# Performance work log

Hardware: AMD Instinct MI355X
Metric: run time of the kernel (lower is better)

## Reference

```python
import jax, jax.numpy as jnp
import numpy as np

NUM_HEADS = 8
EPS = 1e-12  # matches torch F.normalize default eps


def setup_inputs() -> dict:
    key = jax.random.key(0)
    k1, k2 = jax.random.split(key)
    x = jax.random.normal(k1, (8, 384, 128, 128), dtype=jnp.float32)
    # 1x1 conv weight [out=3*dim, in=dim]
    w_qkv = jax.random.normal(k2, (1152, 384), dtype=jnp.float32) * (1.0 / np.sqrt(384))
    return {"x": x, "w_qkv": w_qkv}


def _l2norm(t):
    # torch F.normalize(dim=-1): x / max(||x||2, eps)
    n = jnp.sqrt(jnp.sum(t * t, axis=-1, keepdims=True))
    return t / jnp.maximum(n, EPS)


def reference(x, w_qkv):
    B, C, H, W = x.shape
    hw = H * W
    head_c = C // NUM_HEADS
    # 1x1 conv == channel matmul
    qkv = jnp.einsum('bchw,oc->bohw', x, w_qkv)  # [B, 3C, H, W]
    q, k, v = jnp.split(qkv, 3, axis=1)
    def rs(t):
        return t.reshape(B, NUM_HEADS, head_c, hw)
    q, k, v = rs(q), rs(k), rs(v)
    q = _l2norm(q)
    k = _l2norm(k)
    scale = jnp.sqrt(jnp.float32(hw))
    attn = jnp.einsum('bhcn,bhdn->bhcd', q, k) / scale  # small CxC per head
    attn = jax.nn.softmax(attn, axis=-1)
    out = jnp.einsum('bhcd,bhdn->bhcn', attn, v)
    return out.reshape(B, C, H, W)
```

## Files before the change

### kernel.cpp

```cpp
#include <hip/hip_runtime.h>

typedef short short8 __attribute__((ext_vector_type(8)));
typedef __bf16 bf16x8 __attribute__((ext_vector_type(8)));
typedef float f32x4 __attribute__((ext_vector_type(4)));
typedef int i32x4 __attribute__((ext_vector_type(4)));

typedef const __attribute__((address_space(1))) void* gas_p;
typedef __attribute__((address_space(3))) void* las_p;

static __device__ __forceinline__ unsigned short f2bf(float f) {
  unsigned u = __builtin_bit_cast(unsigned, f);
  u += 0x7fffu + ((u >> 16) & 1u);
  return (unsigned short)(u >> 16);
}
static __device__ __forceinline__ float bf2f(unsigned short h) {
  unsigned u = ((unsigned)h) << 16;
  return __builtin_bit_cast(float, u);
}

#define MFMA16(a, b, c) __builtin_amdgcn_mfma_f32_16x16x32_bf16( \
    __builtin_bit_cast(bf16x8, a), __builtin_bit_cast(bf16x8, b), (c), 0, 0, 0)

__global__ __launch_bounds__(64) void k0_wfrag(const float* __restrict__ w,
                                               unsigned short* __restrict__ wfrag) {
  int bx = blockIdx.x;
  int m16 = bx / 12, kb = bx % 12;
  int lane = threadIdx.x;
  int i = lane & 15, g = lane >> 4;
  int o = m16 * 16 + i;
  int k = kb * 32 + g * 8;
  const float* src = w + (size_t)o * 384 + k;
  f32x4 f0 = *(const f32x4*)(src);
  f32x4 f1 = *(const f32x4*)(src + 4);
  short8 v;
#pragma unroll
  for (int j = 0; j < 4; ++j) { v[j] = (short)f2bf(f0[j]); v[4 + j] = (short)f2bf(f1[j]); }
  *(short8*)(wfrag + ((size_t)(m16 * 12 + kb) * 64 + lane) * 8) = v;
}

__global__ __launch_bounds__(256) void kx_transpose(const float* __restrict__ x,
                                                    unsigned short* __restrict__ xt,
                                                    int bbase) {
  __shared__ unsigned T[64 * 32];
  int n0 = blockIdx.x * 64, c0 = blockIdx.y * 64;
  int bl = blockIdx.z;
  int bg = bbase + bl;
  int t = threadIdx.x;
  int cl2 = t >> 6, nl = t & 63;
  const float* xb = x + ((size_t)bg * 384 + c0) * 16384 + n0 + nl;
#pragma unroll
  for (int u = 0; u < 8; ++u) {
    int cb = cl2 * 2 + u * 8;
    float f0 = xb[(size_t)cb * 16384];
    float f1 = xb[(size_t)(cb + 1) * 16384];
    unsigned p = (unsigned)f2bf(f0) | ((unsigned)f2bf(f1) << 16);
    int cp = cb >> 1;
    T[nl * 32 + (cp ^ (nl & 31))] = p;
  }
  __syncthreads();
  int nl2 = t >> 2, cg = t & 3;
  unsigned vals[8];
#pragma unroll
  for (int j = 0; j < 8; ++j)
    vals[j] = T[nl2 * 32 + ((cg * 8 + j) ^ (nl2 & 31))];
  unsigned short* dst = xt + ((size_t)bl * 16384 + n0 + nl2) * 384 + c0 + cg * 16;
  *(i32x4*)(dst)     = (i32x4){(int)vals[0], (int)vals[1], (int)vals[2], (int)vals[3]};
  *(i32x4*)(dst + 8) = (i32x4){(int)vals[4], (int)vals[5], (int)vals[6], (int)vals[7]};
}

__global__ __launch_bounds__(256, 4) void k1_qkv(const unsigned short* __restrict__ xt,
                                                 const unsigned short* __restrict__ wfrag,
                                                 unsigned short* __restrict__ qkv,
                                                 float* __restrict__ norms2,
                                                 int bbase, int nb) {
  __shared__ union {
    unsigned short Bt[2][128 * 32];
    unsigned short Cl[128 * 136];
  } sm;

  int flat = blockIdx.x;
  int b_l = flat % nb;
  int rem = flat / nb;
  int m = rem % 9, ntile = rem / 9;
  int o0 = m * 128, n0 = ntile * 128;
  int bg = bbase + b_l;
  int t = threadIdx.x;
  int wave = t >> 6, lane = t & 63;
  int i = lane & 15, g = lane >> 4;
  int mh = wave >> 1, nh = wave & 1;

  const unsigned short* xrow = xt + ((size_t)b_l * 16384 + n0 + (t >> 2)) * 384 + (t & 3) * 8;

  f32x4 acc[4][4];
#pragma unroll
  for (int a = 0; a < 4; ++a)
#pragma unroll
    for (int c = 0; c < 4; ++c) acc[a][c] = (f32x4){0.f, 0.f, 0.f, 0.f};

#define STAGE(buf, kb)                                                          \
  do {                                                                          \
    const unsigned short* s0 = xrow + (kb) * 32;                                \
    unsigned short* d0 = &sm.Bt[0][0] + (buf) * 4096 + t * 8;                   \
    __builtin_amdgcn_global_load_lds((gas_p)s0, (las_p)d0, 16, 0, 0);           \
    __builtin_amdgcn_global_load_lds((gas_p)(s0 + (size_t)64 * 384),            \
                                     (las_p)(d0 + 2048), 16, 0, 0);             \
  } while (0)

  STAGE(0, 0);
  for (int kb = 0; kb < 12; ++kb) {
    __syncthreads();
    if (kb < 11) STAGE((kb + 1) & 1, kb + 1);
    short8 aF[4];
#pragma unroll
    for (int mt = 0; mt < 4; ++mt)
      aF[mt] = *(const short8*)(wfrag + ((size_t)((m * 8 + mh * 4 + mt) * 12 + kb) * 64 + lane) * 8);
    const unsigned short* bbaseL = &sm.Bt[kb & 1][(nh * 64) * 32 + g * 8];
#pragma unroll
    for (int nt = 0; nt < 4; ++nt) {
      short8 bF = *(const short8*)(bbaseL + (nt * 16 + i) * 32);
#pragma unroll
      for (int mt = 0; mt < 4; ++mt) acc[mt][nt] = MFMA16(aF[mt], bF, acc[mt][nt]);
    }
  }
#undef STAGE

  __syncthreads();

#pragma unroll
  for (int mt = 0; mt < 4; ++mt)
#pragma unroll
    for (int nt = 0; nt < 4; ++nt)
#pragma unroll
      for (int rr = 0; rr < 4; ++rr)
        sm.Cl[(mh * 64 + mt * 16 + 4 * g + rr) * 136 + nh * 64 + nt * 16 + i] =
            f2bf(acc[mt][nt][rr]);
  __syncthreads();

  size_t obase = ((size_t)bg * 1152 + o0) * 16384 + n0;
  int srow = t >> 4, scol = (t & 15) * 8;
#pragma unroll
  for (int u = 0; u < 8; ++u) {
    int row = u * 16 + srow;
    short8 vv = *(const short8*)&sm.Cl[row * 136 + scol];
    *(short8*)(qkv + obase + (size_t)row * 16384 + scol) = vv;
  }

  if (o0 < 768) {
    int row = t >> 1, half = t & 1;
    const unsigned short* p = &sm.Cl[row * 136 + half * 64];
    float s = 0.f;
#pragma unroll
    for (int u = 0; u < 8; ++u) {
      short8 vv = *(const short8*)(p + u * 8);
#pragma unroll
      for (int e = 0; e < 8; ++e) {
        float f = bf2f((unsigned short)vv[e]);
        s += f * f;
      }
    }
    s += __shfl_xor(s, 1, 64);
    if (half == 0) atomicAdd(&norms2[bg * 768 + o0 + row], s);
  }
}

__global__ __launch_bounds__(256) void k2_gram(const unsigned short* __restrict__ qkv,
                                               float* __restrict__ G) {
  __shared__ float Gl[48 * 48];
  int bh = blockIdx.x >> 4, chunk = blockIdx.x & 15;
  int b = bh >> 3, hi = bh & 7;
  int t = threadIdx.x, wave = t >> 6, lane = t & 63;
  int i = lane & 15, g = lane >> 4;
  for (int u = t; u < 2304; u += 256) Gl[u] = 0.f;
  __syncthreads();

  const unsigned short* qbase = qkv + ((size_t)b * 1152 + hi * 48) * 16384;
  const unsigned short* kbase = qbase + (size_t)384 * 16384;
  int pos0 = chunk * 1024 + wave * 256;

  f32x4 acc[3][3];
#pragma unroll
  for (int a = 0; a < 3; ++a)
#pragma unroll
    for (int c = 0; c < 3; ++c) acc[a][c] = (f32x4){0.f, 0.f, 0.f, 0.f};

  for (int ks = 0; ks < 8; ++ks) {
    int kp = pos0 + ks * 32 + g * 8;
    short8 aF[3], bF[3];
#pragma unroll
    for (int mt = 0; mt < 3; ++mt)
      aF[mt] = *(const short8*)(qbase + (size_t)(mt * 16 + i) * 16384 + kp);
#pragma unroll
    for (int nt = 0; nt < 3; ++nt)
      bF[nt] = *(const short8*)(kbase + (size_t)(nt * 16 + i) * 16384 + kp);
#pragma unroll
    for (int mt = 0; mt < 3; ++mt)
#pragma unroll
      for (int nt = 0; nt < 3; ++nt) acc[mt][nt] = MFMA16(aF[mt], bF[nt], acc[mt][nt]);
  }
#pragma unroll
  for (int mt = 0; mt < 3; ++mt)
#pragma unroll
    for (int nt = 0; nt < 3; ++nt)
#pragma unroll
      for (int rr = 0; rr < 4; ++rr)
        atomicAdd(&Gl[(mt * 16 + 4 * g + rr) * 48 + nt * 16 + i], acc[mt][nt][rr]);
  __syncthreads();
  float* Gg = G + (size_t)bh * 2304;
  for (int u = t; u < 2304; u += 256) atomicAdd(&Gg[u], Gl[u]);
}

__global__ __launch_bounds__(64) void k2b_softmax(const float* __restrict__ G,
                                                  const float* __restrict__ norms2,
                                                  float* __restrict__ attn) {
  int bh = blockIdx.x;
  int b = bh >> 3, hi = bh & 7;
  int c = threadIdx.x;
  if (c >= 48) return;
  const float* Gg = G + (size_t)bh * 2304 + c * 48;
  const float* nq = norms2 + b * 768 + hi * 48;
  const float* nk = nq + 384;
  float dq = fmaxf(sqrtf(nq[c]), 1e-12f);
  float l[48];
  float m = -1e30f;
#pragma unroll
  for (int d = 0; d < 48; ++d) {
    float dk = fmaxf(sqrtf(nk[d]), 1e-12f);
    l[d] = Gg[d] / (dq * dk * 128.0f);
    m = fmaxf(m, l[d]);
  }
  float s = 0.f;
#pragma unroll
  for (int d = 0; d < 48; ++d) {
    l[d] = expf(l[d] - m);
    s += l[d];
  }
  float inv = 1.0f / s;
  float* A = attn + (size_t)bh * 2304 + c * 48;
#pragma unroll
  for (int d = 0; d < 48; ++d) A[d] = l[d] * inv;
}

__global__ __launch_bounds__(256) void k3_out(const unsigned short* __restrict__ qkv,
                                              const float* __restrict__ attn,
                                              float* __restrict__ out) {
  __shared__ unsigned short Vt[256 * 72];
  int nchunk = blockIdx.x, bh = blockIdx.y;
  int b = bh >> 3, hi = bh & 7;
  int n0 = nchunk * 256;
  int t = threadIdx.x, wave = t >> 6, lane = t & 63;
  int i = lane & 15, g = lane >> 4;

  const unsigned short* vbase = qkv + ((size_t)b * 1152 + 768 + hi * 48) * 16384 + n0 + t;
  unsigned short* vr = &Vt[t * 72];
#pragma unroll
  for (int dp = 0; dp < 24; ++dp) {
    unsigned a0 = vbase[(size_t)(2 * dp) * 16384];
    unsigned a1 = vbase[(size_t)(2 * dp + 1) * 16384];
    *(unsigned*)(vr + 2 * dp) = a0 | (a1 << 16);
  }
  *(i32x4*)(vr + 48) = (i32x4){0, 0, 0, 0};
  *(i32x4*)(vr + 56) = (i32x4){0, 0, 0, 0};

  const float* Ab = attn + (size_t)bh * 2304;
  short8 aF[3][2];
#pragma unroll
  for (int mt = 0; mt < 3; ++mt) {
    int row = mt * 16 + i;
    f32x4 f0 = *(const f32x4*)(Ab + row * 48 + 8 * g);
    f32x4 f1 = *(const f32x4*)(Ab + row * 48 + 8 * g + 4);
    short8 a0;
#pragma unroll
    for (int j = 0; j < 4; ++j) { a0[j] = (short)f2bf(f0[j]); a0[4 + j] = (short)f2bf(f1[j]); }
    aF[mt][0] = a0;
    short8 a1v = (short8){0, 0, 0, 0, 0, 0, 0, 0};
    if (g < 2) {
      f32x4 h0 = *(const f32x4*)(Ab + row * 48 + 32 + 8 * g);
      f32x4 h1 = *(const f32x4*)(Ab + row * 48 + 32 + 8 * g + 4);
#pragma unroll
      for (int j = 0; j < 4; ++j) { a1v[j] = (short)f2bf(h0[j]); a1v[4 + j] = (short)f2bf(h1[j]); }
    }
    aF[mt][1] = a1v;
  }
  __syncthreads();

  f32x4 acc[3][4];
#pragma unroll
  for (int a = 0; a < 3; ++a)
#pragma unroll
    for (int c = 0; c < 4; ++c) acc[a][c] = (f32x4){0.f, 0.f, 0.f, 0.f};

  int nb = wave * 64;
#pragma unroll
  for (int nt = 0; nt < 4; ++nt) {
    const unsigned short* vp = &Vt[(size_t)(nb + nt * 16 + i) * 72 + 8 * g];
    short8 b0 = *(const short8*)vp;
    short8 b1 = *(const short8*)(vp + 32);
#pragma unroll
    for (int mt = 0; mt < 3; ++mt) {
      acc[mt][nt] = MFMA16(aF[mt][0], b0, acc[mt][nt]);
      acc[mt][nt] = MFMA16(aF[mt][1], b1, acc[mt][nt]);
    }
  }

  float* ob = out + ((size_t)b * 384 + hi * 48) * 16384 + n0 + nb;
#pragma unroll
  for (int mt = 0; mt < 3; ++mt)
#pragma unroll
    for (int nt = 0; nt < 4; ++nt)
#pragma unroll
      for (int rr = 0; rr < 4; ++rr)
        ob[(size_t)(mt * 16 + 4 * g + rr) * 16384 + nt * 16 + i] = acc[mt][nt][rr];
}

extern "C" void kernel_launch(void* const* d_in, const int* in_sizes, int n_in,
                              void* d_out, int out_size, void* d_ws, size_t ws_size,
                              hipStream_t stream) {
  const float* x = (const float*)d_in[0];
  const float* w = (const float*)d_in[1];
  float* out = (float*)d_out;
  char* ws = (char*)d_ws;

  unsigned short* qkv   = (unsigned short*)(ws);
  unsigned short* wfrag = (unsigned short*)(ws + 301989888LL);
  float* norms2         = (float*)(ws + 302874624LL);
  float* G              = (float*)(ws + 302899200LL);
  float* attn           = (float*)(ws + 303489024LL);
  unsigned short* xtb   = (unsigned short*)(ws + 304078848LL);

  const size_t FULL_NEED = 304078848LL + 100663296LL;

  hipMemsetAsync(ws + 302874624LL, 0, 24576 + 589824, stream);
  k0_wfrag<<<864, 64, 0, stream>>>(w, wfrag);

  if (ws_size >= FULL_NEED) {
    kx_transpose<<<dim3(256, 6, 8), 256, 0, stream>>>(x, xtb, 0);
    k1_qkv<<<9216, 256, 0, stream>>>(xtb, wfrag, qkv, norms2, 0, 8);
  } else {
    for (int b = 0; b < 8; ++b) {
      kx_transpose<<<dim3(256, 6, 1), 256, 0, stream>>>(x, xtb, b);
      k1_qkv<<<1152, 256, 0, stream>>>(xtb, wfrag, qkv, norms2, b, 1);
    }
  }

  k2_gram<<<1024, 256, 0, stream>>>(qkv, G);
  k2b_softmax<<<64, 64, 0, stream>>>(G, norms2, attn);
  k3_out<<<dim3(64, 64), 256, 0, stream>>>(qkv, attn, out);
}
```

Before: 390.1 us.

## Swizzle LDS tile, prefetch weight fragments, fuse softmax into gram via last-block counter

Three separate changes. In the QKV GEMM, the LDS staging layout is XOR-swizzled to cut bank conflicts on fragment reads, and the weight fragments for the next k-step are loaded after the current MFMAs so global latency overlaps compute. Separately, the softmax kernel is folded into the gram kernel: each chunk block bumps a per-head atomic counter and the last one computes the softmax, which removes a launch. This adds threadfences and a counter buffer, and it shifts the workspace offsets.

```diff
diff --git a/kernel.cpp b/kernel.cpp
--- a/kernel.cpp
+++ b/kernel.cpp
@@ -89,7 +89,12 @@
   int i = lane & 15, g = lane >> 4;
   int mh = wave >> 1, nh = wave & 1;
 
-  const unsigned short* xrow = xt + ((size_t)b_l * 16384 + n0 + (t >> 2)) * 384 + (t & 3) * 8;
+  int r = t >> 2, blk = t & 3;
+  int srcblk = blk ^ (r & 3);
+  const unsigned short* xrow =
+      xt + ((size_t)b_l * 16384 + n0 + r) * 384 + srcblk * 8;
+
+  const unsigned short* wbase = wfrag + ((size_t)(m * 8 + mh * 4) * 12 * 64 + lane) * 8;
 
   f32x4 acc[4][4];
 #pragma unroll
@@ -106,20 +111,27 @@
                                      (las_p)(d0 + 2048), 16, 0, 0);             \
   } while (0)
 
+  short8 aF[4];
+#pragma unroll
+  for (int mt = 0; mt < 4; ++mt)
+    aF[mt] = *(const short8*)(wbase + (size_t)(mt * 12) * 512);
   STAGE(0, 0);
+
   for (int kb = 0; kb < 12; ++kb) {
     __syncthreads();
     if (kb < 11) STAGE((kb + 1) & 1, kb + 1);
-    short8 aF[4];
-#pragma unroll
-    for (int mt = 0; mt < 4; ++mt)
-      aF[mt] = *(const short8*)(wfrag + ((size_t)((m * 8 + mh * 4 + mt) * 12 + kb) * 64 + lane) * 8);
-    const unsigned short* bbaseL = &sm.Bt[kb & 1][(nh * 64) * 32 + g * 8];
+    const unsigned short* bb = &sm.Bt[kb & 1][0];
+    int swz = (g ^ (i & 3)) * 8;
 #pragma unroll
     for (int nt = 0; nt < 4; ++nt) {
-      short8 bF = *(const short8*)(bbaseL + (nt * 16 + i) * 32);
+      short8 bF = *(const short8*)(bb + (nh * 64 + nt * 16 + i) * 32 + swz);
 #pragma unroll
       for (int mt = 0; mt < 4; ++mt) acc[mt][nt] = MFMA16(aF[mt], bF, acc[mt][nt]);
+    }
+    if (kb < 11) {
+#pragma unroll
+      for (int mt = 0; mt < 4; ++mt)
+        aF[mt] = *(const short8*)(wbase + (size_t)(mt * 12 + kb + 1) * 512);
     }
   }
 #undef STAGE
@@ -164,8 +176,12 @@
 }
 
 __global__ __launch_bounds__(256) void k2_gram(const unsigned short* __restrict__ qkv,
-                                               float* __restrict__ G) {
+                                               float* __restrict__ G,
+                                               const float* __restrict__ norms2,
+                                               float* __restrict__ attn,
+                                               int* __restrict__ cnt) {
   __shared__ float Gl[48 * 48];
+  __shared__ int sDone;
   int bh = blockIdx.x >> 4, chunk = blockIdx.x & 15;
   int b = bh >> 3, hi = bh & 7;
   int t = threadIdx.x, wave = t >> 6, lane = t & 63;
@@ -207,31 +223,30 @@
   __syncthreads();
   float* Gg = G + (size_t)bh * 2304;
   for (int u = t; u < 2304; u += 256) atomicAdd(&Gg[u], Gl[u]);
-}
-
-__global__ __launch_bounds__(64) void k2b_softmax(const float* __restrict__ G,
-                                                  const float* __restrict__ norms2,
-                                                  float* __restrict__ attn) {
-  int bh = blockIdx.x;
-  int b = bh >> 3, hi = bh & 7;
-  int c = threadIdx.x;
+
+  __threadfence();
+  if (t == 0) sDone = atomicAdd(&cnt[bh], 1);
+  __syncthreads();
+  if (sDone != 15) return;
+  __threadfence();
+  int c = t;
   if (c >= 48) return;
-  const float* Gg = G + (size_t)bh * 2304 + c * 48;
   const float* nq = norms2 + b * 768 + hi * 48;
   const float* nk = nq + 384;
   float dq = fmaxf(sqrtf(nq[c]), 1e-12f);
+  const float* Gr = Gg + c * 48;
   float l[48];
-  float m = -1e30f;
+  float mx = -1e30f;
 #pragma unroll
   for (int d = 0; d < 48; ++d) {
     float dk = fmaxf(sqrtf(nk[d]), 1e-12f);
-    l[d] = Gg[d] / (dq * dk * 128.0f);
-    m = fmaxf(m, l[d]);
+    l[d] = Gr[d] / (dq * dk * 128.0f);
+    mx = fmaxf(mx, l[d]);
   }
   float s = 0.f;
 #pragma unroll
   for (int d = 0; d < 48; ++d) {
-    l[d] = expf(l[d] - m);
+    l[d] = expf(l[d] - mx);
     s += l[d];
   }
   float inv = 1.0f / s;
@@ -324,12 +339,13 @@
   unsigned short* wfrag = (unsigned short*)(ws + 301989888LL);
   float* norms2         = (float*)(ws + 302874624LL);
   float* G              = (float*)(ws + 302899200LL);
-  float* attn           = (float*)(ws + 303489024LL);
-  unsigned short* xtb   = (unsigned short*)(ws + 304078848LL);
-
-  const size_t FULL_NEED = 304078848LL + 100663296LL;
-
-  hipMemsetAsync(ws + 302874624LL, 0, 24576 + 589824, stream);
+  int*   cnt            = (int*)(ws + 303489024LL);
+  float* attn           = (float*)(ws + 303489280LL);
+  unsigned short* xtb   = (unsigned short*)(ws + 304079104LL);
+
+  const size_t FULL_NEED = 304079104LL + 100663296LL;
+
+  hipMemsetAsync(ws + 302874624LL, 0, 24576 + 589824 + 256, stream);
   k0_wfrag<<<864, 64, 0, stream>>>(w, wfrag);
 
   if (ws_size >= FULL_NEED) {
@@ -342,7 +358,6 @@
     }
   }
 
-  k2_gram<<<1024, 256, 0, stream>>>(qkv, G);
-  k2b_softmax<<<64, 64, 0, stream>>>(G, norms2, attn);
+  k2_gram<<<1024, 256, 0, stream>>>(qkv, G, norms2, attn, cnt);
   k3_out<<<dim3(64, 64), 256, 0, stream>>>(qkv, attn, out);
 }
```

Measured after the change: 475.3 us. 1.22x slower.
